# Kernel optimization log

Measured on AMD Instinct MI355X. Metric: run time of the kernel, lower is better.

Reference implementation:

```python
import jax, jax.numpy as jnp
import numpy as np

N_NODES = 100000
N_EDGES = 6400000
IN_DIM = 128
HIDDEN = 16
P_DROP = 0.3
LN_EPS = 1e-5


def setup_inputs() -> dict:
    key = jax.random.key(0)
    ks = jax.random.split(key, 6)
    x = jax.random.normal(ks[0], (N_NODES, IN_DIM), dtype=jnp.float32)
    edge_index = jax.random.randint(ks[1], (2, N_EDGES), 0, N_NODES, dtype=jnp.int32)
    gamma = jnp.ones((IN_DIM,), dtype=jnp.float32)
    beta = jnp.zeros((IN_DIM,), dtype=jnp.float32)
    W1 = jax.random.normal(ks[2], (IN_DIM, HIDDEN), dtype=jnp.float32) / np.sqrt(IN_DIM)
    b1 = jnp.zeros((HIDDEN,), dtype=jnp.float32)
    W2 = jax.random.normal(ks[3], (HIDDEN, HIDDEN), dtype=jnp.float32) / np.sqrt(HIDDEN)
    b2 = jnp.zeros((HIDDEN,), dtype=jnp.float32)
    return {"x": x, "edge_index": edge_index, "gamma": gamma, "beta": beta,
            "W1": W1, "b1": b1, "W2": W2, "b2": b2}


def _gcn_conv(h, W, b, src, dst, norm):
    # linear transform first (hidden is small), then normalized scatter-add
    h = h @ W                                   # [N, F_out]
    msgs = h[src] * norm[:, None]               # gather by source, scale
    out = jax.ops.segment_sum(msgs, dst, num_segments=N_NODES)
    return out + b


def _dropout(h, key):
    keep = jax.random.uniform(key, h.shape) >= P_DROP
    return jnp.where(keep, h / (1.0 - P_DROP), 0.0)


def reference(x, edge_index, gamma, beta, W1, b1, W2, b2):
    # LayerNorm over feature dim
    mu = jnp.mean(x, axis=-1, keepdims=True)
    var = jnp.mean(jnp.square(x - mu), axis=-1, keepdims=True)
    xn = (x - mu) * jax.lax.rsqrt(var + LN_EPS) * gamma + beta

    # PyG GCNConv normalization: add self-loops, sym deg^-1/2 norm
    loops = jnp.arange(N_NODES, dtype=edge_index.dtype)
    src = jnp.concatenate([edge_index[0], loops])
    dst = jnp.concatenate([edge_index[1], loops])
    deg = jax.ops.segment_sum(jnp.ones_like(src, dtype=xn.dtype), dst,
                              num_segments=N_NODES)
    dinv = jax.lax.rsqrt(deg)                   # deg >= 1 (self-loops)
    norm = dinv[src] * dinv[dst]                # [E + N]

    dk1, dk2 = jax.random.split(jax.random.key(42))
    h = jax.nn.relu(_gcn_conv(xn, W1, b1, src, dst, norm))
    h = _dropout(h, dk1)
    h = jax.nn.relu(_gcn_conv(h, W2, b2, src, dst, norm))
    h = _dropout(h, dk2)
    return h
```

## Files before the change

### kernel.cpp

```cpp
#include <hip/hip_runtime.h>
#include <hip/hip_fp16.h>
#include <stdint.h>
#include <stddef.h>

#define N_NODES 100000
#define N_EDGES 6400000
#define HIDDEN 16
#define NBKT 782
#define CAP 8704
#define P1_EPB 8192
#define NMASK 1600000

typedef _Float16 f16x8 __attribute__((ext_vector_type(8)));
typedef _Float16 f16x4 __attribute__((ext_vector_type(4)));
typedef float f32x4 __attribute__((ext_vector_type(4)));

__host__ __device__ inline uint32_t rotl32(uint32_t x, int n) {
    return (x << n) | (x >> (32 - n));
}

__host__ __device__ inline void threefry2x32(uint32_t k0, uint32_t k1,
                                             uint32_t x0, uint32_t x1,
                                             uint32_t& o0, uint32_t& o1) {
    uint32_t k2 = k0 ^ k1 ^ 0x1BD11BDAu;
    x0 += k0; x1 += k1;
    x0 += x1; x1 = rotl32(x1, 13); x1 ^= x0;
    x0 += x1; x1 = rotl32(x1, 15); x1 ^= x0;
    x0 += x1; x1 = rotl32(x1, 26); x1 ^= x0;
    x0 += x1; x1 = rotl32(x1,  6); x1 ^= x0;
    x0 += k1; x1 += k2 + 1u;
    x0 += x1; x1 = rotl32(x1, 17); x1 ^= x0;
    x0 += x1; x1 = rotl32(x1, 29); x1 ^= x0;
    x0 += x1; x1 = rotl32(x1, 16); x1 ^= x0;
    x0 += x1; x1 = rotl32(x1, 24); x1 ^= x0;
    x0 += k2; x1 += k0 + 2u;
    x0 += x1; x1 = rotl32(x1, 13); x1 ^= x0;
    x0 += x1; x1 = rotl32(x1, 15); x1 ^= x0;
    x0 += x1; x1 = rotl32(x1, 26); x1 ^= x0;
    x0 += x1; x1 = rotl32(x1,  6); x1 ^= x0;
    x0 += k0; x1 += k1 + 3u;
    x0 += x1; x1 = rotl32(x1, 17); x1 ^= x0;
    x0 += x1; x1 = rotl32(x1, 29); x1 ^= x0;
    x0 += x1; x1 = rotl32(x1, 16); x1 ^= x0;
    x0 += x1; x1 = rotl32(x1, 24); x1 ^= x0;
    x0 += k1; x1 += k2 + 4u;
    x0 += x1; x1 = rotl32(x1, 13); x1 ^= x0;
    x0 += x1; x1 = rotl32(x1, 15); x1 ^= x0;
    x0 += x1; x1 = rotl32(x1, 26); x1 ^= x0;
    x0 += x1; x1 = rotl32(x1,  6); x1 ^= x0;
    x0 += k2; x1 += k0 + 5u;
    o0 = x0; o1 = x1;
}

__global__ __launch_bounds__(256) void dropmask_kernel(uint64_t* __restrict__ m1,
                                                       uint64_t* __restrict__ m2,
                                                       uint32_t k10, uint32_t k11,
                                                       uint32_t k20, uint32_t k21) {
    int g = blockIdx.x * blockDim.x + threadIdx.x;
    int lane = threadIdx.x & 63;
    bool first = g < NMASK;
    uint32_t j = first ? (uint32_t)g : (uint32_t)(g - NMASK);
    uint32_t a, b;
    threefry2x32(first ? k10 : k20, first ? k11 : k21, 0u, j, a, b);
    uint32_t bits = a ^ b;
    float u = __uint_as_float((bits >> 9) | 0x3F800000u) - 1.0f;
    unsigned long long m = __ballot(u >= 0.3f);
    if (lane == 0) {
        int gw = g >> 6;
        if (first) m1[gw] = m;
        else       m2[gw - (NMASK >> 6)] = m;
    }
}

__global__ void initcur_kernel(int* __restrict__ gcursor) {
    int b = threadIdx.x;
    if (b < NBKT) gcursor[b] = b * CAP;
}

__global__ __launch_bounds__(512) void part1_kernel(const int* __restrict__ src,
                                                    const int* __restrict__ dst,
                                                    int* __restrict__ gcursor,
                                                    int* __restrict__ buf) {
    __shared__ int lhist[NBKT], lbase[NBKT], lstart[NBKT], lcur[NBKT];
    __shared__ int wsum[8];
    __shared__ int lsort[P1_EPB];
    int tid = threadIdx.x;
    const int NV4 = N_EDGES >> 2;
    int base4 = blockIdx.x * (P1_EPB >> 2);
    const int4* dst4 = (const int4*)dst;
    const int4* src4 = (const int4*)src;

    for (int b = tid; b < NBKT; b += 512) lhist[b] = 0;
    __syncthreads();
    #pragma unroll
    for (int i = 0; i < 4; i++) {
        int e4 = base4 + i * 512 + tid;
        if (e4 < NV4) {
            int4 d = dst4[e4];
            atomicAdd(&lhist[d.x >> 7], 1);
            atomicAdd(&lhist[d.y >> 7], 1);
            atomicAdd(&lhist[d.z >> 7], 1);
            atomicAdd(&lhist[d.w >> 7], 1);
        }
    }
    __syncthreads();
    int i0 = tid * 2, i1 = i0 + 1;
    int c0 = (i0 < NBKT) ? lhist[i0] : 0;
    int c1 = (i1 < NBKT) ? lhist[i1] : 0;
    int v = c0 + c1;
    int lane = tid & 63, wid = tid >> 6;
    int sc = v;
    #pragma unroll
    for (int o = 1; o < 64; o <<= 1) {
        int t2 = __shfl_up(sc, o, 64);
        if (lane >= o) sc += t2;
    }
    if (lane == 63) wsum[wid] = sc;
    __syncthreads();
    int wo = 0;
    #pragma unroll
    for (int w = 0; w < 8; w++) wo += (w < wid) ? wsum[w] : 0;
    int excl = sc - v + wo;
    if (i0 < NBKT) { lstart[i0] = excl;      lcur[i0] = excl; }
    if (i1 < NBKT) { lstart[i1] = excl + c0; lcur[i1] = excl + c0; }
    for (int b = tid; b < NBKT; b += 512) {
        int c = lhist[b];
        lbase[b] = c ? atomicAdd(&gcursor[b], c) : 0;
    }
    __syncthreads();
    #pragma unroll
    for (int i = 0; i < 4; i++) {
        int e4 = base4 + i * 512 + tid;
        if (e4 < NV4) {
            int4 d = dst4[e4];
            int4 s = src4[e4];
            int p0 = atomicAdd(&lcur[d.x >> 7], 1);
            lsort[p0] = ((d.x & 127) << 17) | s.x;
            int p1 = atomicAdd(&lcur[d.y >> 7], 1);
            lsort[p1] = ((d.y & 127) << 17) | s.y;
            int p2 = atomicAdd(&lcur[d.z >> 7], 1);
            lsort[p2] = ((d.z & 127) << 17) | s.z;
            int p3 = atomicAdd(&lcur[d.w >> 7], 1);
            lsort[p3] = ((d.w & 127) << 17) | s.w;
        }
    }
    __syncthreads();
    int grp = tid >> 4, gl = tid & 15;
    for (int b = grp; b < NBKT; b += 32) {
        int st = lstart[b], c = lhist[b], gb = lbase[b];
        int lim = (b + 1) * CAP;
        for (int k = gl; k < c; k += 16) {
            int pos = gb + k;
            if (pos < lim)
                buf[pos] = lsort[st + k];
        }
    }
}

__global__ __launch_bounds__(512) void part2_kernel(const int* __restrict__ gcursor,
                                                    int* __restrict__ buf,
                                                    int* __restrict__ nodeinfo,
                                                    float* __restrict__ dinv) {
    __shared__ int lcnt[128], lcur[128];
    __shared__ int w0sum;
    __shared__ int lsort[CAP];
    int b = blockIdx.x, tid = threadIdx.x;
    int base = b * CAP;
    int end = gcursor[b];
    int count = end - base;
    int cnt4 = count >> 2;
    const int4* buf4 = (const int4*)(buf + base);
    if (tid < 128) lcnt[tid] = 0;
    __syncthreads();
    for (int i = tid; i < cnt4; i += 512) {
        int4 w = buf4[i];
        atomicAdd(&lcnt[w.x >> 17], 1);
        atomicAdd(&lcnt[w.y >> 17], 1);
        atomicAdd(&lcnt[w.z >> 17], 1);
        atomicAdd(&lcnt[w.w >> 17], 1);
    }
    for (int i = (cnt4 << 2) + tid; i < count; i += 512)
        atomicAdd(&lcnt[buf[base + i] >> 17], 1);
    __syncthreads();
    if (tid < 128) {
        int v = lcnt[tid];
        int lane = tid & 63;
        int sc = v;
        #pragma unroll
        for (int o = 1; o < 64; o <<= 1) {
            int t2 = __shfl_up(sc, o, 64);
            if (lane >= o) sc += t2;
        }
        if (tid == 63) w0sum = sc;
        __syncthreads();
        int incl = sc + ((tid >= 64) ? w0sum : 0);
        int excl = incl - v;
        lcur[tid] = excl;
        int n = b * 128 + tid;
        if (n < N_NODES) {
            nodeinfo[n] = (v << 23) | (base + excl);
            dinv[n] = rsqrtf((float)v + 1.0f);
        }
    } else {
        __syncthreads();
    }
    __syncthreads();
    for (int i = tid; i < cnt4; i += 512) {
        int4 w = buf4[i];
        int p0 = atomicAdd(&lcur[w.x >> 17], 1); lsort[p0] = w.x & 0x1FFFF;
        int p1 = atomicAdd(&lcur[w.y >> 17], 1); lsort[p1] = w.y & 0x1FFFF;
        int p2 = atomicAdd(&lcur[w.z >> 17], 1); lsort[p2] = w.z & 0x1FFFF;
        int p3 = atomicAdd(&lcur[w.w >> 17], 1); lsort[p3] = w.w & 0x1FFFF;
    }
    for (int i = (cnt4 << 2) + tid; i < count; i += 512) {
        int w = buf[base + i];
        int pos = atomicAdd(&lcur[w >> 17], 1);
        lsort[pos] = w & 0x1FFFF;
    }
    __syncthreads();
    int4* bufw4 = (int4*)(buf + base);
    const int4* lsort4 = (const int4*)lsort;
    for (int i = tid; i < cnt4; i += 512) bufw4[i] = lsort4[i];
    for (int i = (cnt4 << 2) + tid; i < count; i += 512) buf[base + i] = lsort[i];
}

#define XSTR 136
__global__ __launch_bounds__(256) void ln_w1_kernel(const float* __restrict__ x,
                             const float* __restrict__ gamma,
                             const float* __restrict__ beta,
                             const float* __restrict__ W1,
                             const float* __restrict__ dinv,
                             __half* __restrict__ g1) {
    __shared__ __align__(16) _Float16 xnh[64 * XSTR];
    __shared__ __align__(16) _Float16 w1t[16 * XSTR];
    int tid = threadIdx.x;

    {
        int n = tid & 15, kb = tid >> 4;
        f16x8 wv;
        #pragma unroll
        for (int j = 0; j < 8; j++)
            wv[j] = (_Float16)W1[(kb * 8 + j) * 16 + n];
        *(f16x8*)&w1t[n * XSTR + kb * 8] = wv;
    }

    const float4* xt = (const float4*)x;
    size_t base4 = (size_t)blockIdx.x * 2048;
    const size_t NF4 = (size_t)N_NODES * 32;
    float4 v[8];
    #pragma unroll
    for (int j = 0; j < 8; j++) {
        size_t idx = base4 + (size_t)j * 256 + tid;
        v[j] = (idx < NF4) ? xt[idx] : make_float4(0.f, 0.f, 0.f, 0.f);
    }
    int col = tid & 31;
    int sub = tid >> 5;
    float4 gv = ((const float4*)gamma)[col];
    float4 bv = ((const float4*)beta)[col];
    #pragma unroll
    for (int j = 0; j < 8; j++) {
        float s1 = v[j].x + v[j].y + v[j].z + v[j].w;
        float s2 = v[j].x * v[j].x + v[j].y * v[j].y
                 + v[j].z * v[j].z + v[j].w * v[j].w;
        #pragma unroll
        for (int o = 1; o < 32; o <<= 1) {
            s1 += __shfl_xor(s1, o, 64);
            s2 += __shfl_xor(s2, o, 64);
        }
        float mu = s1 * (1.0f / 128.0f);
        float var = s2 * (1.0f / 128.0f) - mu * mu;
        float rstd = rsqrtf(var + 1e-5f);
        int row = j * 8 + sub;
        f16x4 h;
        h[0] = (_Float16)((v[j].x - mu) * rstd * gv.x + bv.x);
        h[1] = (_Float16)((v[j].y - mu) * rstd * gv.y + bv.y);
        h[2] = (_Float16)((v[j].z - mu) * rstd * gv.z + bv.z);
        h[3] = (_Float16)((v[j].w - mu) * rstd * gv.w + bv.w);
        *(f16x4*)&xnh[row * XSTR + col * 4] = h;
    }
    __syncthreads();

    int l = tid & 63, w = tid >> 6;
    int am = l & 15, ak = l >> 4;
    const _Float16* abase = &xnh[(w * 16 + am) * XSTR + ak * 8];
    const _Float16* bbase = &w1t[am * XSTR + ak * 8];
    f32x4 acc = {0.f, 0.f, 0.f, 0.f};
    #pragma unroll
    for (int kk = 0; kk < 4; kk++) {
        f16x8 av = *(const f16x8*)(abase + kk * 32);
        f16x8 bv2 = *(const f16x8*)(bbase + kk * 32);
        acc = __builtin_amdgcn_mfma_f32_16x16x32_f16(av, bv2, acc, 0, 0, 0);
    }
    _Float16* g1h = (_Float16*)g1;
    #pragma unroll
    for (int reg = 0; reg < 4; reg++) {
        int row = w * 16 + ak * 4 + reg;
        int nn = blockIdx.x * 64 + row;
        if (nn < N_NODES)
            g1h[nn * 16 + am] = (_Float16)(acc[reg] * dinv[nn]);
    }
}

__global__ __launch_bounds__(256) void pull1_kernel(const int* __restrict__ nodeinfo,
                             const int* __restrict__ sorted_src,
                             const __half* __restrict__ g1,
                             const float* __restrict__ dinv,
                             const float* __restrict__ b1,
                             const float* __restrict__ W2,
                             const uint64_t* __restrict__ m1,
                             __half* __restrict__ g2) {
    __shared__ float sW2[HIDDEN * HIDDEN];
    sW2[threadIdx.x] = W2[threadIdx.x];
    __syncthreads();
    int n = blockIdx.x * 16 + (threadIdx.x >> 4);
    int l = threadIdx.x & 15;
    int c2 = l & 1, e8 = l >> 1;
    const _Float16* gt = (const _Float16*)g1;
    int info = nodeinfo[n];
    int start = info & 0x7FFFFF;
    int deg = (int)((unsigned)info >> 23);

    float acc[8] = {0.f,0.f,0.f,0.f,0.f,0.f,0.f,0.f};
    float acc2[8] = {0.f,0.f,0.f,0.f,0.f,0.f,0.f,0.f};
    if (e8 == 0) {
        f16x8 sv = *(const f16x8*)(gt + (uint32_t)n * 16 + c2 * 8);
        #pragma unroll
        for (int j = 0; j < 8; j++) acc[j] = (float)sv[j];
    }
    int km = (deg > 0) ? deg - 1 : 0;
    for (int kb = 0; kb < deg; kb += 16) {
        int k0 = kb + e8, k1 = kb + 8 + e8;
        int s0 = sorted_src[start + min(k0, km)];
        int s1 = sorted_src[start + min(k1, km)];
        if (k0 < deg) {
            f16x8 gv = *(const f16x8*)(gt + (uint32_t)s0 * 16 + c2 * 8);
            #pragma unroll
            for (int j = 0; j < 8; j++) acc[j] += (float)gv[j];
        }
        if (k1 < deg) {
            f16x8 gv = *(const f16x8*)(gt + (uint32_t)s1 * 16 + c2 * 8);
            #pragma unroll
            for (int j = 0; j < 8; j++) acc2[j] += (float)gv[j];
        }
    }
    #pragma unroll
    for (int j = 0; j < 8; j++) acc[j] += acc2[j];
    float h4[4];
    {
        int sel = e8 & 1;
        #pragma unroll
        for (int j = 0; j < 4; j++) {
            float mine = sel ? acc[j + 4] : acc[j];
            float give = sel ? acc[j] : acc[j + 4];
            h4[j] = mine + __shfl_xor(give, 2, 64);
        }
    }
    float h2[2];
    {
        int sel = (e8 >> 1) & 1;
        #pragma unroll
        for (int j = 0; j < 2; j++) {
            float mine = sel ? h4[j + 2] : h4[j];
            float give = sel ? h4[j] : h4[j + 2];
            h2[j] = mine + __shfl_xor(give, 4, 64);
        }
    }
    float hv;
    {
        int sel = (e8 >> 2) & 1;
        float mine = sel ? h2[1] : h2[0];
        float give = sel ? h2[0] : h2[1];
        hv = mine + __shfl_xor(give, 8, 64);
    }
    int cc = c2 * 8 + (e8 & 1) * 4 + ((e8 >> 1) & 1) * 2 + ((e8 >> 2) & 1);
    float di = dinv[n];
    uint32_t mbits = (uint32_t)(m1[n >> 2] >> ((n & 3) * 16));
    float hd = ((mbits >> cc) & 1)
             ? fmaxf(di * hv + b1[cc], 0.f) * (1.0f / 0.7f) : 0.f;
    int grpbase = threadIdx.x & 48;
    int c = l & 3;
    float4 o4 = make_float4(0.f, 0.f, 0.f, 0.f);
    #pragma unroll
    for (int i = 0; i < 16; i++) {
        int srcl = grpbase + (((i >> 3) & 1) | (((i >> 2) & 1) << 1) |
                              (((i >> 1) & 1) << 2) | ((i & 1) << 3));
        float hi = __shfl(hd, srcl, 64);
        const float4 w = *(const float4*)&sW2[i * HIDDEN + c * 4];
        o4.x += hi * w.x; o4.y += hi * w.y; o4.z += hi * w.z; o4.w += hi * w.w;
    }
    if (l < 4) {
        __half2 p0 = __floats2half2_rn(o4.x * di, o4.y * di);
        __half2 p1 = __floats2half2_rn(o4.z * di, o4.w * di);
        uint2 u;
        u.x = *(uint32_t*)&p0; u.y = *(uint32_t*)&p1;
        *(uint2*)((__half*)g2 + (uint32_t)n * 16 + c * 4) = u;
    }
}

__global__ __launch_bounds__(256) void pull2_kernel(const int* __restrict__ nodeinfo,
                             const int* __restrict__ sorted_src,
                             const __half* __restrict__ g2,
                             const float* __restrict__ dinv,
                             const float* __restrict__ b2,
                             const uint64_t* __restrict__ m2,
                             float* __restrict__ out) {
    int n = blockIdx.x * 16 + (threadIdx.x >> 4);
    int l = threadIdx.x & 15;
    int c2 = l & 1, e8 = l >> 1;
    const _Float16* gt = (const _Float16*)g2;
    int info = nodeinfo[n];
    int start = info & 0x7FFFFF;
    int deg = (int)((unsigned)info >> 23);

    float acc[8] = {0.f,0.f,0.f,0.f,0.f,0.f,0.f,0.f};
    float acc2[8] = {0.f,0.f,0.f,0.f,0.f,0.f,0.f,0.f};
    if (e8 == 0) {
        f16x8 sv = *(const f16x8*)(gt + (uint32_t)n * 16 + c2 * 8);
        #pragma unroll
        for (int j = 0; j < 8; j++) acc[j] = (float)sv[j];
    }
    int km = (deg > 0) ? deg - 1 : 0;
    for (int kb = 0; kb < deg; kb += 16) {
        int k0 = kb + e8, k1 = kb + 8 + e8;
        int s0 = sorted_src[start + min(k0, km)];
        int s1 = sorted_src[start + min(k1, km)];
        if (k0 < deg) {
            f16x8 gv = *(const f16x8*)(gt + (uint32_t)s0 * 16 + c2 * 8);
            #pragma unroll
            for (int j = 0; j < 8; j++) acc[j] += (float)gv[j];
        }
        if (k1 < deg) {
            f16x8 gv = *(const f16x8*)(gt + (uint32_t)s1 * 16 + c2 * 8);
            #pragma unroll
            for (int j = 0; j < 8; j++) acc2[j] += (float)gv[j];
        }
    }
    #pragma unroll
    for (int j = 0; j < 8; j++) acc[j] += acc2[j];
    float h4[4];
    {
        int sel = e8 & 1;
        #pragma unroll
        for (int j = 0; j < 4; j++) {
            float mine = sel ? acc[j + 4] : acc[j];
            float give = sel ? acc[j] : acc[j + 4];
            h4[j] = mine + __shfl_xor(give, 2, 64);
        }
    }
    float h2[2];
    {
        int sel = (e8 >> 1) & 1;
        #pragma unroll
        for (int j = 0; j < 2; j++) {
            float mine = sel ? h4[j + 2] : h4[j];
            float give = sel ? h4[j] : h4[j + 2];
            h2[j] = mine + __shfl_xor(give, 4, 64);
        }
    }
    float hv;
    {
        int sel = (e8 >> 2) & 1;
        float mine = sel ? h2[1] : h2[0];
        float give = sel ? h2[0] : h2[1];
        hv = mine + __shfl_xor(give, 8, 64);
    }
    int cc = c2 * 8 + (e8 & 1) * 4 + ((e8 >> 1) & 1) * 2 + ((e8 >> 2) & 1);
    float di = dinv[n];
    uint32_t mbits = (uint32_t)(m2[n >> 2] >> ((n & 3) * 16));
    float r = ((mbits >> cc) & 1)
            ? fmaxf(di * hv + b2[cc], 0.f) * (1.0f / 0.7f) : 0.f;
    out[(uint32_t)n * 16 + cc] = r;
}

extern "C" void kernel_launch(void* const* d_in, const int* in_sizes, int n_in,
                              void* d_out, int out_size, void* d_ws, size_t ws_size,
                              hipStream_t stream) {
    const float* x     = (const float*)d_in[0];
    const int*   ei    = (const int*)d_in[1];
    const float* gamma = (const float*)d_in[2];
    const float* beta  = (const float*)d_in[3];
    const float* W1    = (const float*)d_in[4];
    const float* b1    = (const float*)d_in[5];
    const float* W2    = (const float*)d_in[6];
    const float* b2    = (const float*)d_in[7];
    float* out = (float*)d_out;
    const int* src = ei;
    const int* dst = ei + N_EDGES;

    uint32_t dk1_0, dk1_1, dk2_0, dk2_1;
    threefry2x32(0u, 42u, 0u, 0u, dk1_0, dk1_1);
    threefry2x32(0u, 42u, 0u, 1u, dk2_0, dk2_1);

    int*      gcursor  = (int*)d_ws;
    int*      nodeinfo = gcursor + 1024;
    float*    dinv     = (float*)(nodeinfo + N_NODES);
    int*      buf      = (int*)(dinv + N_NODES);
    __half*   g1h      = (__half*)(buf + (size_t)NBKT * CAP);
    __half*   g2h      = g1h + (size_t)N_NODES * HIDDEN;
    uint64_t* m1       = (uint64_t*)(g2h + (size_t)N_NODES * HIDDEN);
    uint64_t* m2       = m1 + (NMASK >> 6);

    const int NB_LN = (N_NODES + 63) / 64;
    const int NB_PULL = N_NODES / 16;
    const int NB_P1 = (N_EDGES + P1_EPB - 1) / P1_EPB;

    initcur_kernel<<<1, 1024, 0, stream>>>(gcursor);
    dropmask_kernel<<<(2 * NMASK) / 256, 256, 0, stream>>>(m1, m2,
                                                           dk1_0, dk1_1,
                                                           dk2_0, dk2_1);
    part1_kernel<<<NB_P1, 512, 0, stream>>>(src, dst, gcursor, buf);
    part2_kernel<<<NBKT, 512, 0, stream>>>(gcursor, buf, nodeinfo, dinv);
    ln_w1_kernel<<<NB_LN, 256, 0, stream>>>(x, gamma, beta, W1, dinv, g1h);
    pull1_kernel<<<NB_PULL, 256, 0, stream>>>(nodeinfo, buf, g1h,
                                              dinv, b1, W2, m1, g2h);
    pull2_kernel<<<NB_PULL, 256, 0, stream>>>(nodeinfo, buf, g2h,
                                              dinv, b2, m2, out);
}
```

Measured before the change: 283.4 us.

## Fuse dropout RNG into pull kernels and pack partition histograms to shrink LDS

```diff
diff --git a/kernel.cpp b/kernel.cpp
--- a/kernel.cpp
+++ b/kernel.cpp
@@ -7,9 +7,9 @@
 #define N_EDGES 6400000
 #define HIDDEN 16
 #define NBKT 782
+#define NBKTP 391
 #define CAP 8704
-#define P1_EPB 8192
-#define NMASK 1600000
+#define P1_EPB 6144
 
 typedef _Float16 f16x8 __attribute__((ext_vector_type(8)));
 typedef _Float16 f16x4 __attribute__((ext_vector_type(4)));
@@ -52,24 +52,12 @@
     o0 = x0; o1 = x1;
 }
 
-__global__ __launch_bounds__(256) void dropmask_kernel(uint64_t* __restrict__ m1,
-                                                       uint64_t* __restrict__ m2,
-                                                       uint32_t k10, uint32_t k11,
-                                                       uint32_t k20, uint32_t k21) {
-    int g = blockIdx.x * blockDim.x + threadIdx.x;
-    int lane = threadIdx.x & 63;
-    bool first = g < NMASK;
-    uint32_t j = first ? (uint32_t)g : (uint32_t)(g - NMASK);
+__device__ inline bool keep_bit(uint32_t k0, uint32_t k1, uint32_t j) {
     uint32_t a, b;
-    threefry2x32(first ? k10 : k20, first ? k11 : k21, 0u, j, a, b);
+    threefry2x32(k0, k1, 0u, j, a, b);
     uint32_t bits = a ^ b;
     float u = __uint_as_float((bits >> 9) | 0x3F800000u) - 1.0f;
-    unsigned long long m = __ballot(u >= 0.3f);
-    if (lane == 0) {
-        int gw = g >> 6;
-        if (first) m1[gw] = m;
-        else       m2[gw - (NMASK >> 6)] = m;
-    }
+    return u >= 0.3f;
 }
 
 __global__ void initcur_kernel(int* __restrict__ gcursor) {
@@ -81,7 +69,9 @@
                                                     const int* __restrict__ dst,
                                                     int* __restrict__ gcursor,
                                                     int* __restrict__ buf) {
-    __shared__ int lhist[NBKT], lbase[NBKT], lstart[NBKT], lcur[NBKT];
+    __shared__ uint32_t lhistp[NBKTP];
+    __shared__ uint32_t lcurp[NBKTP];
+    __shared__ int lbase[NBKT];
     __shared__ int wsum[8];
     __shared__ int lsort[P1_EPB];
     int tid = threadIdx.x;
@@ -90,23 +80,23 @@
     const int4* dst4 = (const int4*)dst;
     const int4* src4 = (const int4*)src;
 
-    for (int b = tid; b < NBKT; b += 512) lhist[b] = 0;
-    __syncthreads();
-    #pragma unroll
-    for (int i = 0; i < 4; i++) {
+    if (tid < NBKTP) lhistp[tid] = 0;
+    __syncthreads();
+    #pragma unroll
+    for (int i = 0; i < 3; i++) {
         int e4 = base4 + i * 512 + tid;
         if (e4 < NV4) {
             int4 d = dst4[e4];
-            atomicAdd(&lhist[d.x >> 7], 1);
-            atomicAdd(&lhist[d.y >> 7], 1);
-            atomicAdd(&lhist[d.z >> 7], 1);
-            atomicAdd(&lhist[d.w >> 7], 1);
-        }
-    }
-    __syncthreads();
-    int i0 = tid * 2, i1 = i0 + 1;
-    int c0 = (i0 < NBKT) ? lhist[i0] : 0;
-    int c1 = (i1 < NBKT) ? lhist[i1] : 0;
+            int b0 = d.x >> 7, b1 = d.y >> 7, b2 = d.z >> 7, b3 = d.w >> 7;
+            atomicAdd(&lhistp[b0 >> 1], 1u << ((b0 & 1) << 4));
+            atomicAdd(&lhistp[b1 >> 1], 1u << ((b1 & 1) << 4));
+            atomicAdd(&lhistp[b2 >> 1], 1u << ((b2 & 1) << 4));
+            atomicAdd(&lhistp[b3 >> 1], 1u << ((b3 & 1) << 4));
+        }
+    }
+    __syncthreads();
+    uint32_t pk = (tid < NBKTP) ? lhistp[tid] : 0u;
+    int c0 = pk & 0xFFFF, c1 = pk >> 16;
     int v = c0 + c1;
     int lane = tid & 63, wid = tid >> 6;
     int sc = v;
@@ -121,33 +111,39 @@
     #pragma unroll
     for (int w = 0; w < 8; w++) wo += (w < wid) ? wsum[w] : 0;
     int excl = sc - v + wo;
-    if (i0 < NBKT) { lstart[i0] = excl;      lcur[i0] = excl; }
-    if (i1 < NBKT) { lstart[i1] = excl + c0; lcur[i1] = excl + c0; }
-    for (int b = tid; b < NBKT; b += 512) {
-        int c = lhist[b];
-        lbase[b] = c ? atomicAdd(&gcursor[b], c) : 0;
-    }
-    __syncthreads();
-    #pragma unroll
-    for (int i = 0; i < 4; i++) {
+    if (tid < NBKTP) {
+        lcurp[tid] = ((uint32_t)(excl + c0) << 16) | (uint32_t)excl;
+        if (c0) lbase[2 * tid]     = atomicAdd(&gcursor[2 * tid], c0);
+        if (c1) lbase[2 * tid + 1] = atomicAdd(&gcursor[2 * tid + 1], c1);
+    }
+    __syncthreads();
+    #pragma unroll
+    for (int i = 0; i < 3; i++) {
         int e4 = base4 + i * 512 + tid;
         if (e4 < NV4) {
             int4 d = dst4[e4];
             int4 s = src4[e4];
-            int p0 = atomicAdd(&lcur[d.x >> 7], 1);
-            lsort[p0] = ((d.x & 127) << 17) | s.x;
-            int p1 = atomicAdd(&lcur[d.y >> 7], 1);
-            lsort[p1] = ((d.y & 127) << 17) | s.y;
-            int p2 = atomicAdd(&lcur[d.z >> 7], 1);
-            lsort[p2] = ((d.z & 127) << 17) | s.z;
-            int p3 = atomicAdd(&lcur[d.w >> 7], 1);
-            lsort[p3] = ((d.w & 127) << 17) | s.w;
+            int b0 = d.x >> 7; int sh0 = (b0 & 1) << 4;
+            uint32_t o0 = atomicAdd(&lcurp[b0 >> 1], 1u << sh0);
+            lsort[(o0 >> sh0) & 0xFFFF] = ((d.x & 127) << 17) | s.x;
+            int b1 = d.y >> 7; int sh1 = (b1 & 1) << 4;
+            uint32_t o1 = atomicAdd(&lcurp[b1 >> 1], 1u << sh1);
+            lsort[(o1 >> sh1) & 0xFFFF] = ((d.y & 127) << 17) | s.y;
+            int b2 = d.z >> 7; int sh2 = (b2 & 1) << 4;
+            uint32_t o2 = atomicAdd(&lcurp[b2 >> 1], 1u << sh2);
+            lsort[(o2 >> sh2) & 0xFFFF] = ((d.z & 127) << 17) | s.z;
+            int b3 = d.w >> 7; int sh3 = (b3 & 1) << 4;
+            uint32_t o3 = atomicAdd(&lcurp[b3 >> 1], 1u << sh3);
+            lsort[(o3 >> sh3) & 0xFFFF] = ((d.w & 127) << 17) | s.w;
         }
     }
     __syncthreads();
     int grp = tid >> 4, gl = tid & 15;
     for (int b = grp; b < NBKT; b += 32) {
-        int st = lstart[b], c = lhist[b], gb = lbase[b];
+        int sh = (b & 1) << 4;
+        int c   = (lhistp[b >> 1] >> sh) & 0xFFFF;
+        int end = (lcurp[b >> 1]  >> sh) & 0xFFFF;
+        int st = end - c, gb = lbase[b];
         int lim = (b + 1) * CAP;
         for (int k = gl; k < c; k += 16) {
             int pos = gb + k;
@@ -307,7 +303,7 @@
                              const float* __restrict__ dinv,
                              const float* __restrict__ b1,
                              const float* __restrict__ W2,
-                             const uint64_t* __restrict__ m1,
+                             uint32_t k10, uint32_t k11,
                              __half* __restrict__ g2) {
     __shared__ float sW2[HIDDEN * HIDDEN];
     sW2[threadIdx.x] = W2[threadIdx.x];
@@ -374,9 +370,8 @@
     }
     int cc = c2 * 8 + (e8 & 1) * 4 + ((e8 >> 1) & 1) * 2 + ((e8 >> 2) & 1);
     float di = dinv[n];
-    uint32_t mbits = (uint32_t)(m1[n >> 2] >> ((n & 3) * 16));
-    float hd = ((mbits >> cc) & 1)
-             ? fmaxf(di * hv + b1[cc], 0.f) * (1.0f / 0.7f) : 0.f;
+    bool kp = keep_bit(k10, k11, (uint32_t)(n * 16 + cc));
+    float hd = kp ? fmaxf(di * hv + b1[cc], 0.f) * (1.0f / 0.7f) : 0.f;
     int grpbase = threadIdx.x & 48;
     int c = l & 3;
     float4 o4 = make_float4(0.f, 0.f, 0.f, 0.f);
@@ -402,7 +397,7 @@
                              const __half* __restrict__ g2,
                              const float* __restrict__ dinv,
                              const float* __restrict__ b2,
-                             const uint64_t* __restrict__ m2,
+                             uint32_t k20, uint32_t k21,
                              float* __restrict__ out) {
     int n = blockIdx.x * 16 + (threadIdx.x >> 4);
     int l = threadIdx.x & 15;
@@ -466,9 +461,8 @@
     }
     int cc = c2 * 8 + (e8 & 1) * 4 + ((e8 >> 1) & 1) * 2 + ((e8 >> 2) & 1);
     float di = dinv[n];
-    uint32_t mbits = (uint32_t)(m2[n >> 2] >> ((n & 3) * 16));
-    float r = ((mbits >> cc) & 1)
-            ? fmaxf(di * hv + b2[cc], 0.f) * (1.0f / 0.7f) : 0.f;
+    bool kp = keep_bit(k20, k21, (uint32_t)(n * 16 + cc));
+    float r = kp ? fmaxf(di * hv + b2[cc], 0.f) * (1.0f / 0.7f) : 0.f;
     out[(uint32_t)n * 16 + cc] = r;
 }
 
@@ -497,22 +491,17 @@
     int*      buf      = (int*)(dinv + N_NODES);
     __half*   g1h      = (__half*)(buf + (size_t)NBKT * CAP);
     __half*   g2h      = g1h + (size_t)N_NODES * HIDDEN;
-    uint64_t* m1       = (uint64_t*)(g2h + (size_t)N_NODES * HIDDEN);
-    uint64_t* m2       = m1 + (NMASK >> 6);
 
     const int NB_LN = (N_NODES + 63) / 64;
     const int NB_PULL = N_NODES / 16;
     const int NB_P1 = (N_EDGES + P1_EPB - 1) / P1_EPB;
 
     initcur_kernel<<<1, 1024, 0, stream>>>(gcursor);
-    dropmask_kernel<<<(2 * NMASK) / 256, 256, 0, stream>>>(m1, m2,
-                                                           dk1_0, dk1_1,
-                                                           dk2_0, dk2_1);
     part1_kernel<<<NB_P1, 512, 0, stream>>>(src, dst, gcursor, buf);
     part2_kernel<<<NBKT, 512, 0, stream>>>(gcursor, buf, nodeinfo, dinv);
     ln_w1_kernel<<<NB_LN, 256, 0, stream>>>(x, gamma, beta, W1, dinv, g1h);
     pull1_kernel<<<NB_PULL, 256, 0, stream>>>(nodeinfo, buf, g1h,
-                                              dinv, b1, W2, m1, g2h);
+                                              dinv, b1, W2, dk1_0, dk1_1, g2h);
     pull2_kernel<<<NB_PULL, 256, 0, stream>>>(nodeinfo, buf, g2h,
-                                              dinv, b2, m2, out);
-}
+                                              dinv, b2, dk2_0, dk2_1, out);
+}
```

Result: slower. 297.4 us (+5.0%).
